# Performance work log

Measured on AMD Instinct MI355X. Metric: run time of the kernel, lower is better.

The kernel has to match this reference:

```python
import jax, jax.numpy as jnp
import numpy as np

B, IN_DIM, R_DIM = 8192, 2048, 4096
LEAK_RATE = 0.3


def setup_inputs() -> dict:
    key = jax.random.key(0)
    k1, k2, k3, k4 = jax.random.split(key, 4)
    inputs = jax.random.normal(k1, (B, IN_DIM), dtype=jnp.float32)
    prev_state = jax.random.normal(k2, (B, R_DIM), dtype=jnp.float32)
    # weights scaled down for numerical sanity inside tanh
    input_weights = jax.random.normal(k3, (R_DIM, IN_DIM), dtype=jnp.float32) * 0.02
    reservoir_weights = jax.random.normal(k4, (R_DIM, R_DIM), dtype=jnp.float32) * 0.02
    return {
        "inputs": inputs,
        "prev_state": prev_state,
        "input_weights": input_weights,
        "reservoir_weights": reservoir_weights,
    }


def reference(inputs, prev_state, input_weights, reservoir_weights):
    # input_part = inputs @ input_weights.T        -> [B, R]
    # reservoir_part = prev_state @ reservoir_weights.T -> [B, R]
    input_part = jnp.einsum("bi,ri->br", inputs, input_weights)
    reservoir_part = jnp.einsum("bq,rq->br", prev_state, reservoir_weights)
    state = (1.0 - LEAK_RATE) * prev_state + LEAK_RATE * jnp.tanh(input_part + reservoir_part)
    return state
```

## Files before the change

### kernel.cpp

```cpp
#include <hip/hip_runtime.h>
#include <cstdint>
#include <cstddef>

typedef unsigned short u16;
typedef __attribute__((ext_vector_type(8))) short short8;
typedef __attribute__((ext_vector_type(4))) float f32x4;
typedef __attribute__((ext_vector_type(4))) int i32x4;

constexpr int M  = 8192;
constexpr int Nn = 4096;
constexpr int K1 = 2048;
constexpr int K2 = 4096;
constexpr int K  = K1 + K2;
constexpr int BM = 256, BN = 256, BK = 32;
constexpr int NT = K / BK;
constexpr float LEAK = 0.3f;

__device__ __forceinline__ u16 f2bf(float f) {
  unsigned u = __float_as_uint(f);
  u += 0x7FFFu + ((u >> 16) & 1u);
  return (u16)(u >> 16);
}

template<int C1, int C2>
__global__ void cast_concat(const float* __restrict__ X, const float* __restrict__ S,
                            u16* __restrict__ out, int rows)
{
  constexpr int C = C1 + C2;
  const size_t total = (size_t)rows * C / 8;
  for (size_t i = blockIdx.x * (size_t)blockDim.x + threadIdx.x; i < total;
       i += (size_t)gridDim.x * blockDim.x) {
    const size_t e = i * 8;
    const int r = (int)(e / C);
    const int c = (int)(e - (size_t)r * C);
    const float* src = (c < C1) ? (X + (size_t)r * C1 + c)
                                : (S + (size_t)r * C2 + (c - C1));
    const float4* s4 = (const float4*)src;
    float4 f0 = s4[0], f1 = s4[1];
    alignas(16) u16 tmp[8];
    tmp[0] = f2bf(f0.x); tmp[1] = f2bf(f0.y); tmp[2] = f2bf(f0.z); tmp[3] = f2bf(f0.w);
    tmp[4] = f2bf(f1.x); tmp[5] = f2bf(f1.y); tmp[6] = f2bf(f1.z); tmp[7] = f2bf(f1.w);
    *(i32x4*)(out + e) = *(i32x4*)tmp;
  }
}

#define LGKM0()  asm volatile("s_waitcnt lgkmcnt(0)" ::: "memory")
#define LGKM12() asm volatile("s_waitcnt lgkmcnt(12)" ::: "memory")

__global__ __launch_bounds__(512, 2) void gemm_fused(
    const u16* __restrict__ A,
    const u16* __restrict__ W,
    const float* __restrict__ prev,
    float* __restrict__ out)
{
  __shared__ u16 LA[3][256 * 32];
  __shared__ u16 LB[3][256 * 32];

  const int tid  = threadIdx.x;
  const int lane = tid & 63;
  const int wid  = tid >> 6;
  const int wr   = wid >> 2;
  const int wc   = wid & 3;

  const int cpx = gridDim.x >> 3;
  const int wg  = ((int)blockIdx.x & 7) * cpx + ((int)blockIdx.x >> 3);
  const int bn  = wg & 15;
  const int bm  = wg >> 4;

  const u16* Ab = A + (size_t)bm * BM * K;
  const u16* Wb = W + (size_t)bn * BN * K;

  const int srow  = tid >> 2;
  const int sslot = tid & 3;
  const int wslot = sslot ^ ((tid >> 3) & 3);
  const size_t g0 = (size_t)srow * K + sslot * 8;
  const size_t g1 = g0 + (size_t)128 * K;
  const int l0 = srow * 32 + wslot * 8;
  const int l1 = l0 + 128 * 32;

  i32x4 sA0, sA1, sB0, sB1;
  auto issue = [&](int t) {
    const u16* ga = Ab + (size_t)t * BK;
    sA0 = *(const i32x4*)(ga + g0);
    sA1 = *(const i32x4*)(ga + g1);
    const u16* gb = Wb + (size_t)t * BK;
    sB0 = *(const i32x4*)(gb + g0);
    sB1 = *(const i32x4*)(gb + g1);
  };
  auto commit = [&](int w) {
    *(i32x4*)(&LA[w][l0]) = sA0;
    *(i32x4*)(&LA[w][l1]) = sA1;
    *(i32x4*)(&LB[w][l0]) = sB0;
    *(i32x4*)(&LB[w][l1]) = sB1;
  };

  const int frow = lane & 15;
  const int shi  = lane >> 4;
  const int slot = shi ^ ((frow >> 1) & 3);
  const int aoff = (wr * 128 + frow) * 32 + slot * 8;
  const int boff = (wc * 64 + frow) * 32 + slot * 8;

  f32x4 acc[8][4];
  #pragma unroll
  for (int m = 0; m < 8; ++m)
    #pragma unroll
    for (int n = 0; n < 4; ++n) acc[m][n] = (f32x4)0.f;

  short8 af[8];
  short8 bfX[4], bfY[4];

  auto step = [&](int t, int bn_, int bw, short8 (&bfC)[4], short8 (&bfN)[4],
                  bool dR, bool dC, bool dI) {
    if (dC) commit(bw);
    __builtin_amdgcn_sched_barrier(0);
    if (dI) issue(t + 3);
    if (dR) {
      #pragma unroll
      for (int n = 0; n < 4; ++n)
        bfN[n] = *(const short8*)(&LB[bn_][boff + n * 512]);
    }
    #pragma unroll
    for (int m = 0; m < 8; ++m) {
      __builtin_amdgcn_s_setprio(1);
      #pragma unroll
      for (int n = 0; n < 4; ++n)
        acc[m][n] = __builtin_amdgcn_mfma_f32_16x16x32_bf16(af[m], bfC[n], acc[m][n], 0, 0, 0);
      __builtin_amdgcn_s_setprio(0);
      if (dR)
        af[m] = *(const short8*)(&LA[bn_][aoff + m * 512]);
    }
    if (dR) { LGKM12(); } else { LGKM0(); }
    __builtin_amdgcn_s_barrier();
  };

  issue(0); commit(0);
  issue(1); commit(1);
  issue(2);
  LGKM0();
  __builtin_amdgcn_s_barrier();
  #pragma unroll
  for (int m = 0; m < 8; ++m)
    af[m] = *(const short8*)(&LA[0][aoff + m * 512]);
  #pragma unroll
  for (int n = 0; n < 4; ++n)
    bfX[n] = *(const short8*)(&LB[0][boff + n * 512]);

  for (int t6 = 0; t6 < NT - 6; t6 += 6) {
    step(t6 + 0, 1, 2, bfX, bfY, true, true, true);
    step(t6 + 1, 2, 0, bfY, bfX, true, true, true);
    step(t6 + 2, 0, 1, bfX, bfY, true, true, true);
    step(t6 + 3, 1, 2, bfY, bfX, true, true, true);
    step(t6 + 4, 2, 0, bfX, bfY, true, true, true);
    step(t6 + 5, 0, 1, bfY, bfX, true, true, true);
  }
  step(186, 1, 2, bfX, bfY, true,  true,  true);
  step(187, 2, 0, bfY, bfX, true,  true,  true);
  step(188, 0, 1, bfX, bfY, true,  true,  true);
  step(189, 1, 2, bfY, bfX, true,  true,  false);
  step(190, 2, 0, bfX, bfY, true,  false, false);
  step(191, 0, 1, bfY, bfX, false, false, false);

  const int crow0 = bm * BM + wr * 128 + shi * 4;
  const int ccol0 = bn * BN + wc * 64 + frow;
  #pragma unroll
  for (int m = 0; m < 8; ++m)
    #pragma unroll
    for (int n = 0; n < 4; ++n)
      #pragma unroll
      for (int j = 0; j < 4; ++j) {
        const int row = crow0 + m * 16 + j;
        const size_t off = (size_t)row * Nn + ccol0 + n * 16;
        out[off] = (1.0f - LEAK) * prev[off] + LEAK * tanhf(acc[m][n][j]);
      }
}

extern "C" void kernel_launch(void* const* d_in, const int* in_sizes, int n_in,
                              void* d_out, int out_size, void* d_ws, size_t ws_size,
                              hipStream_t stream) {
  const float* inputs = (const float*)d_in[0];
  const float* prev   = (const float*)d_in[1];
  const float* w_in   = (const float*)d_in[2];
  const float* w_res  = (const float*)d_in[3];
  float* out = (float*)d_out;

  u16* Acat = (u16*)d_ws;
  u16* Wcat = Acat + (size_t)M * K;

  cast_concat<K1, K2><<<2048, 256, 0, stream>>>(inputs, prev, Acat, M);
  cast_concat<K1, K2><<<1024, 256, 0, stream>>>(w_in, w_res, Wcat, Nn);

  gemm_fused<<<(M / BM) * (Nn / BN), 512, 0, stream>>>(Acat, Wcat, prev, out);
}
```

Baseline: 509.7 us.

## Rewrite GEMM main loop with direct global-to-LDS loads and BK=64 pipeline

Replaces the register-staged global loads and LDS commits with global_load_lds direct transfers into a swizzled 128KB LDS buffer. The K tile grows to 64, and the loop becomes a ping-pong schedule of quarter-tile MFMA groups interleaved with LDS reads, loads and barriers. The epilogue also swaps tanhf for an exp2/rcp-based fast tanh. The aim is to cut VGPR pressure and LDS-write instruction overhead and to overlap memory with MFMA better. In exchange it adds many barriers, a large LDS footprint that may limit occupancy, and slightly lower tanh accuracy.

```diff
diff --git a/kernel.cpp b/kernel.cpp
--- a/kernel.cpp
+++ b/kernel.cpp
@@ -12,8 +12,8 @@
 constexpr int K1 = 2048;
 constexpr int K2 = 4096;
 constexpr int K  = K1 + K2;
-constexpr int BM = 256, BN = 256, BK = 32;
-constexpr int NT = K / BK;
+constexpr int BM = 256, BN = 256;
+constexpr int NKT = K / 64;
 constexpr float LEAK = 0.3f;
 
 __device__ __forceinline__ u16 f2bf(float f) {
@@ -44,8 +44,24 @@
   }
 }
 
-#define LGKM0()  asm volatile("s_waitcnt lgkmcnt(0)" ::: "memory")
-#define LGKM12() asm volatile("s_waitcnt lgkmcnt(12)" ::: "memory")
+__device__ __forceinline__ void gload16(const u16* g, u16* l) {
+  __builtin_amdgcn_global_load_lds(
+      (const __attribute__((address_space(1))) void*)g,
+      (__attribute__((address_space(3))) void*)l, 16, 0, 0);
+}
+
+__device__ __forceinline__ float fast_tanh(float x) {
+  const float ax = __builtin_fabsf(x);
+  const float e  = __builtin_amdgcn_exp2f(ax * 2.8853900817779268f);
+  const float r  = 1.0f - 2.0f * __builtin_amdgcn_rcpf(e + 1.0f);
+  return __builtin_copysignf(r, x);
+}
+
+#define BAR()   __builtin_amdgcn_s_barrier()
+#define LGKM0() asm volatile("s_waitcnt lgkmcnt(0)" ::: "memory")
+#define VMW4()  asm volatile("s_waitcnt vmcnt(4)" ::: "memory")
+#define VMW0()  asm volatile("s_waitcnt vmcnt(0)" ::: "memory")
+#define SB0()   __builtin_amdgcn_sched_barrier(0)
 
 __global__ __launch_bounds__(512, 2) void gemm_fused(
     const u16* __restrict__ A,
@@ -53,8 +69,7 @@
     const float* __restrict__ prev,
     float* __restrict__ out)
 {
-  __shared__ u16 LA[3][256 * 32];
-  __shared__ u16 LB[3][256 * 32];
+  __shared__ u16 lds[65536];
 
   const int tid  = threadIdx.x;
   const int lane = tid & 63;
@@ -67,101 +82,120 @@
   const int bn  = wg & 15;
   const int bm  = wg >> 4;
 
-  const u16* Ab = A + (size_t)bm * BM * K;
-  const u16* Wb = W + (size_t)bn * BN * K;
-
-  const int srow  = tid >> 2;
-  const int sslot = tid & 3;
-  const int wslot = sslot ^ ((tid >> 3) & 3);
-  const size_t g0 = (size_t)srow * K + sslot * 8;
-  const size_t g1 = g0 + (size_t)128 * K;
-  const int l0 = srow * 32 + wslot * 8;
-  const int l1 = l0 + 128 * 32;
-
-  i32x4 sA0, sA1, sB0, sB1;
-  auto issue = [&](int t) {
-    const u16* ga = Ab + (size_t)t * BK;
-    sA0 = *(const i32x4*)(ga + g0);
-    sA1 = *(const i32x4*)(ga + g1);
-    const u16* gb = Wb + (size_t)t * BK;
-    sB0 = *(const i32x4*)(gb + g0);
-    sB1 = *(const i32x4*)(gb + g1);
-  };
-  auto commit = [&](int w) {
-    *(i32x4*)(&LA[w][l0]) = sA0;
-    *(i32x4*)(&LA[w][l1]) = sA1;
-    *(i32x4*)(&LB[w][l0]) = sB0;
-    *(i32x4*)(&LB[w][l1]) = sB1;
-  };
-
-  const int frow = lane & 15;
-  const int shi  = lane >> 4;
-  const int slot = shi ^ ((frow >> 1) & 3);
-  const int aoff = (wr * 128 + frow) * 32 + slot * 8;
-  const int boff = (wc * 64 + frow) * 32 + slot * 8;
-
-  f32x4 acc[8][4];
+  const int sr = tid >> 3;
+  const int ss = (tid & 7) ^ (sr & 7);
+  const u16* pA = A + (size_t)(bm * BM + sr) * K + ss * 8;
+  const u16* pW = W + (size_t)(bn * BN + sr) * K + ss * 8;
+  u16* ldsw = lds + wid * 512;
+  const size_t rowK64  = (size_t)64  * K;
+  const size_t rowK128 = (size_t)128 * K;
+
+  auto stg = [&](const u16* g, int dst) {
+    gload16(g,          ldsw + dst);
+    gload16(g + rowK64, ldsw + dst + 4096);
+  };
+
+  const int fr  = lane & 15;
+  const int khi = lane >> 4;
+  const int lx  = lane & 7;
+  const int aoff0 = wr * 8192 + fr * 64 + ((khi    ) ^ lx) * 8;
+  const int aoff1 = wr * 8192 + fr * 64 + ((4 + khi) ^ lx) * 8;
+  const int brow  = (wc & 1) * 64 + fr;
+  const int boff0 = (wc >> 1) * 8192 + brow * 64 + ((khi    ) ^ lx) * 8;
+  const int boff1 = (wc >> 1) * 8192 + brow * 64 + ((4 + khi) ^ lx) * 8;
+
+  short8 af[4][2], bf[4][2];
+  f32x4  acc[8][4];
   #pragma unroll
   for (int m = 0; m < 8; ++m)
     #pragma unroll
     for (int n = 0; n < 4; ++n) acc[m][n] = (f32x4)0.f;
 
-  short8 af[8];
-  short8 bfX[4], bfY[4];
-
-  auto step = [&](int t, int bn_, int bw, short8 (&bfC)[4], short8 (&bfN)[4],
-                  bool dR, bool dC, bool dI) {
-    if (dC) commit(bw);
-    __builtin_amdgcn_sched_barrier(0);
-    if (dI) issue(t + 3);
-    if (dR) {
+  auto dsA = [&](int mg, int ab) {
+    #pragma unroll
+    for (int mi = 0; mi < 4; ++mi) {
+      af[mi][0] = *(const short8*)(lds + ab + aoff0 + (mg * 4 + mi) * 1024);
+      af[mi][1] = *(const short8*)(lds + ab + aoff1 + (mg * 4 + mi) * 1024);
+    }
+  };
+  auto dsB = [&](int ng, int bb) {
+    #pragma unroll
+    for (int ni = 0; ni < 2; ++ni) {
+      const int n = ng * 2 + ni;
+      bf[n][0] = *(const short8*)(lds + bb + boff0 + n * 1024);
+      bf[n][1] = *(const short8*)(lds + bb + boff1 + n * 1024);
+    }
+  };
+  auto MM = [&](int mg, int ng) {
+    __builtin_amdgcn_s_setprio(1);
+    #pragma unroll
+    for (int ni = 0; ni < 2; ++ni)
       #pragma unroll
-      for (int n = 0; n < 4; ++n)
-        bfN[n] = *(const short8*)(&LB[bn_][boff + n * 512]);
-    }
-    #pragma unroll
-    for (int m = 0; m < 8; ++m) {
-      __builtin_amdgcn_s_setprio(1);
-      #pragma unroll
-      for (int n = 0; n < 4; ++n)
-        acc[m][n] = __builtin_amdgcn_mfma_f32_16x16x32_bf16(af[m], bfC[n], acc[m][n], 0, 0, 0);
-      __builtin_amdgcn_s_setprio(0);
-      if (dR)
-        af[m] = *(const short8*)(&LA[bn_][aoff + m * 512]);
-    }
-    if (dR) { LGKM12(); } else { LGKM0(); }
-    __builtin_amdgcn_s_barrier();
-  };
-
-  issue(0); commit(0);
-  issue(1); commit(1);
-  issue(2);
-  LGKM0();
-  __builtin_amdgcn_s_barrier();
-  #pragma unroll
-  for (int m = 0; m < 8; ++m)
-    af[m] = *(const short8*)(&LA[0][aoff + m * 512]);
-  #pragma unroll
-  for (int n = 0; n < 4; ++n)
-    bfX[n] = *(const short8*)(&LB[0][boff + n * 512]);
-
-  for (int t6 = 0; t6 < NT - 6; t6 += 6) {
-    step(t6 + 0, 1, 2, bfX, bfY, true, true, true);
-    step(t6 + 1, 2, 0, bfY, bfX, true, true, true);
-    step(t6 + 2, 0, 1, bfX, bfY, true, true, true);
-    step(t6 + 3, 1, 2, bfY, bfX, true, true, true);
-    step(t6 + 4, 2, 0, bfX, bfY, true, true, true);
-    step(t6 + 5, 0, 1, bfY, bfX, true, true, true);
+      for (int mi = 0; mi < 4; ++mi)
+        #pragma unroll
+        for (int ks = 0; ks < 2; ++ks)
+          acc[mg * 4 + mi][ng * 2 + ni] = __builtin_amdgcn_mfma_f32_16x16x32_bf16(
+              af[mi][ks], bf[ng * 2 + ni][ks], acc[mg * 4 + mi][ng * 2 + ni], 0, 0, 0);
+    __builtin_amdgcn_s_setprio(0);
+  };
+
+  stg(pW,                32768);
+  stg(pW + rowK128,      32768 + 8192);
+  stg(pA,                0);
+  stg(pA + rowK128,      8192);
+  stg(pW + 64,           49152);
+  stg(pW + 64 + rowK128, 49152 + 8192);
+  VMW4();
+  BAR();
+
+  const u16* gA = pA;
+  const u16* gW = pW;
+  #pragma unroll 1
+  for (int i = 0; i < NKT / 2 - 1; ++i) {
+    dsA(0, 0); dsB(0, 32768);
+    stg(gA + 64, 16384);
+    BAR(); LGKM0(); SB0(); MM(0, 0); BAR();
+    dsB(1, 32768);
+    stg(gA + 64 + rowK128, 16384 + 8192);
+    BAR(); LGKM0(); SB0(); MM(0, 1); BAR();
+    dsA(1, 0);
+    stg(gW + 128, 32768);
+    BAR(); LGKM0(); SB0(); MM(1, 0); BAR();
+    stg(gW + 128 + rowK128, 32768 + 8192);
+    BAR(); MM(1, 1); VMW4(); BAR();
+    dsA(0, 16384); dsB(0, 49152);
+    stg(gA + 128, 0);
+    BAR(); LGKM0(); SB0(); MM(0, 0); BAR();
+    dsB(1, 49152);
+    stg(gA + 128 + rowK128, 8192);
+    BAR(); LGKM0(); SB0(); MM(0, 1); BAR();
+    dsA(1, 16384);
+    stg(gW + 192, 49152);
+    BAR(); LGKM0(); SB0(); MM(1, 0); BAR();
+    stg(gW + 192 + rowK128, 49152 + 8192);
+    BAR(); MM(1, 1); VMW4(); BAR();
+    gA += 128; gW += 128;
   }
-  step(186, 1, 2, bfX, bfY, true,  true,  true);
-  step(187, 2, 0, bfY, bfX, true,  true,  true);
-  step(188, 0, 1, bfX, bfY, true,  true,  true);
-  step(189, 1, 2, bfY, bfX, true,  true,  false);
-  step(190, 2, 0, bfX, bfY, true,  false, false);
-  step(191, 0, 1, bfY, bfX, false, false, false);
-
-  const int crow0 = bm * BM + wr * 128 + shi * 4;
-  const int ccol0 = bn * BN + wc * 64 + frow;
+
+  dsA(0, 0); dsB(0, 32768);
+  stg(gA + 64, 16384);
+  BAR(); LGKM0(); SB0(); MM(0, 0); BAR();
+  dsB(1, 32768);
+  stg(gA + 64 + rowK128, 16384 + 8192);
+  BAR(); LGKM0(); SB0(); MM(0, 1); BAR();
+  dsA(1, 0);
+  BAR(); LGKM0(); SB0(); MM(1, 0); BAR();
+  BAR(); MM(1, 1); VMW0(); BAR();
+  dsA(0, 16384); dsB(0, 49152);
+  BAR(); LGKM0(); SB0(); MM(0, 0); BAR();
+  dsB(1, 49152);
+  BAR(); LGKM0(); SB0(); MM(0, 1); BAR();
+  dsA(1, 16384);
+  BAR(); LGKM0(); SB0(); MM(1, 0); BAR();
+  BAR(); MM(1, 1);
+
+  const int crow0 = bm * BM + wr * 128 + khi * 4;
+  const int ccol0 = bn * BN + wc * 64 + fr;
   #pragma unroll
   for (int m = 0; m < 8; ++m)
     #pragma unroll
@@ -170,7 +204,7 @@
       for (int j = 0; j < 4; ++j) {
         const int row = crow0 + m * 16 + j;
         const size_t off = (size_t)row * Nn + ccol0 + n * 16;
-        out[off] = (1.0f - LEAK) * prev[off] + LEAK * tanhf(acc[m][n][j]);
+        out[off] = (1.0f - LEAK) * prev[off] + LEAK * fast_tanh(acc[m][n][j]);
       }
 }
 
```

Result: faster. 433.6 us (-14.9%).
